# Kernel optimization log

Hardware: AMD Instinct MI355X
Metric: run time of the kernel (lower is better)

Reference implementation:

```python
import jax, jax.numpy as jnp
import numpy as np

NHEAD = 8  # matches init_kwargs

M_NODES = 20000
D_MODEL = 512
N_EDGES = 640000


def setup_inputs() -> dict:
    key = jax.random.key(0)
    ks = jax.random.split(key, 8)
    sc = 1.0 / np.sqrt(D_MODEL)
    return {
        "s": jax.random.normal(ks[0], (M_NODES, D_MODEL), dtype=jnp.float32),
        "edge_index": jax.random.randint(ks[1], (2, N_EDGES), 0, M_NODES, dtype=jnp.int64),
        "Wq": jax.random.normal(ks[2], (D_MODEL, D_MODEL), dtype=jnp.float32) * sc,
        "bq": jax.random.normal(ks[3], (D_MODEL,), dtype=jnp.float32) * sc,
        "Wkv": jax.random.normal(ks[4], (2 * D_MODEL, D_MODEL), dtype=jnp.float32) * sc,
        "bkv": jax.random.normal(ks[5], (2 * D_MODEL,), dtype=jnp.float32) * sc,
        "Wo": jax.random.normal(ks[6], (D_MODEL, D_MODEL), dtype=jnp.float32) * sc,
        "bo": jax.random.normal(ks[7], (D_MODEL,), dtype=jnp.float32) * sc,
    }


def reference(s, edge_index, Wq, bq, Wkv, bkv, Wo, bo):
    M, C = s.shape
    H = NHEAD
    Dh = C // H
    scale = 1.0 / np.sqrt(Dh).astype(np.float32)

    q = (s @ Wq.T + bq).reshape(M, H, Dh)            # [M,H,Dh]
    kv = (s @ Wkv.T + bkv).reshape(M, H, 2 * Dh)     # [M,H,2Dh]
    k, v = kv[..., :Dh], kv[..., Dh:]

    src, tgt = edge_index[0], edge_index[1]

    # per-edge attention logits [E,H]
    a = jnp.einsum('ehc,ehc->eh', q[tgt], k[src]) * scale

    # segment softmax over edges sharing the same target node
    a_max = jax.ops.segment_max(a, tgt, num_segments=M)        # [M,H]
    ex = jnp.exp(a - a_max[tgt])                               # [E,H]
    denom = jax.ops.segment_sum(ex, tgt, num_segments=M)      # [M,H]
    attn = ex / denom[tgt]                                     # [E,H]

    # weighted message aggregation: scatter-sum over target nodes
    o_msg = attn[..., None] * v[src]                           # [E,H,Dh]
    o = jax.ops.segment_sum(o_msg, tgt, num_segments=M)       # [M,H,Dh]
    o = o.reshape(M, C)
    return o @ Wo.T + bo
```

## Files before the change

### kernel.cpp

```cpp
#include <hip/hip_runtime.h>
#include <cmath>

#define MN 20000
#define DM 512
#define NE 640000
#define CAP 128

typedef short bf16x8 __attribute__((ext_vector_type(8)));
typedef float f32x4 __attribute__((ext_vector_type(4)));

__device__ __forceinline__ ushort f2b(float x) {
    unsigned u = __builtin_bit_cast(unsigned, x);
    u += 0x7FFF + ((u >> 16) & 1);
    return (ushort)(u >> 16);
}
__device__ __forceinline__ float b2f(ushort b) {
    return __builtin_bit_cast(float, (unsigned)b << 16);
}

__global__ void conv_bf16_k(const float* __restrict__ in, ushort* __restrict__ out, int n4) {
    int i = blockIdx.x * blockDim.x + threadIdx.x;
    if (i >= n4) return;
    float4 v = ((const float4*)in)[i];
    ushort4 o = { f2b(v.x), f2b(v.y), f2b(v.z), f2b(v.w) };
    ((ushort4*)out)[i] = o;
}

__device__ __forceinline__ const float* wc_src_row(int r, const float* Wq, const float* Wkv) {
    if (r < 512) return Wq + ((size_t)r << 9);
    if (r < 1024) { int h = (r - 512) >> 6, j = (r - 512) & 63;  return Wkv + ((size_t)(h * 128 + j) << 9); }
    { int h = (r - 1024) >> 6, j = (r - 1024) & 63; return Wkv + ((size_t)(h * 128 + 64 + j) << 9); }
}

__global__ void conv_wc_k(const float* __restrict__ Wq, const float* __restrict__ Wkv,
                          ushort* __restrict__ out) {
    int i = blockIdx.x * blockDim.x + threadIdx.x;
    if (i >= 1536 * 512 / 4) return;
    int e = i * 4;
    int row = e >> 9, col = e & 511;
    float4 v = *(const float4*)(wc_src_row(row, Wq, Wkv) + col);
    ushort4 o = { f2b(v.x), f2b(v.y), f2b(v.z), f2b(v.w) };
    ((ushort4*)out)[i] = o;
}

__global__ void bias_perm_k(const float* __restrict__ bq, const float* __restrict__ bkv,
                            float* __restrict__ bc) {
    int r = blockIdx.x * blockDim.x + threadIdx.x;
    if (r >= 1536) return;
    float v;
    if (r < 512) v = bq[r];
    else if (r < 1024) { int h = (r - 512) >> 6, j = (r - 512) & 63;  v = bkv[h * 128 + j]; }
    else               { int h = (r - 1024) >> 6, j = (r - 1024) & 63; v = bkv[h * 128 + 64 + j]; }
    bc[r] = v;
}

__global__ void conv_split_k(const float* __restrict__ in, ushort* __restrict__ oh,
                             ushort* __restrict__ ol, int n4) {
    int i = blockIdx.x * blockDim.x + threadIdx.x;
    if (i >= n4) return;
    float4 v = ((const float4*)in)[i];
    ushort4 h, l;
    h.x = f2b(v.x); l.x = f2b(v.x - b2f(h.x));
    h.y = f2b(v.y); l.y = f2b(v.y - b2f(h.y));
    h.z = f2b(v.z); l.z = f2b(v.z - b2f(h.z));
    h.w = f2b(v.w); l.w = f2b(v.w - b2f(h.w));
    ((ushort4*)oh)[i] = h;
    ((ushort4*)ol)[i] = l;
}

template<int SPLIT, bool OUTBF>
__global__ __launch_bounds__(256) void gemm_mfma(
    const ushort* __restrict__ Ah, const ushort* __restrict__ Al,
    const ushort* __restrict__ Bh, const ushort* __restrict__ Bl,
    const float* __restrict__ bias, void* __restrict__ Cout, int M, int N, int K)
{
    __shared__ ushort lds[4 * 4096];
    const int tid = threadIdx.x;
    const int row0 = blockIdx.x * 128, col0 = blockIdx.y * 128;
    const int wid = tid >> 6, l = tid & 63;
    const int wm = (wid >> 1) * 64, wn = (wid & 1) * 64;
    const int fr = l & 15, g = l >> 4;
    const int fcb = g << 4;

    f32x4 acc[4][4] = {};

    for (int k0 = 0; k0 < K; k0 += 32) {
        __syncthreads();
#pragma unroll
        for (int c = 0; c < 2; ++c) {
            const int lb  = c * 4096 + tid * 16;
            const int r   = lb >> 6;
            const int cbs = (lb & 63) ^ ((r & 6) << 3);
            const int ar  = min(row0 + r, M - 1);
            const int br  = col0 + r;
            const size_t aoff = (size_t)ar * K + k0 + (cbs >> 1);
            const size_t boff = (size_t)br * K + k0 + (cbs >> 1);
            __builtin_amdgcn_global_load_lds(
                (const __attribute__((address_space(1))) void*)(Ah + aoff),
                (__attribute__((address_space(3))) void*)&lds[0 * 4096 + (lb >> 1)], 16, 0, 0);
            __builtin_amdgcn_global_load_lds(
                (const __attribute__((address_space(1))) void*)(Bh + boff),
                (__attribute__((address_space(3))) void*)&lds[1 * 4096 + (lb >> 1)], 16, 0, 0);
            if (SPLIT == 3) {
                __builtin_amdgcn_global_load_lds(
                    (const __attribute__((address_space(1))) void*)(Al + aoff),
                    (__attribute__((address_space(3))) void*)&lds[2 * 4096 + (lb >> 1)], 16, 0, 0);
                __builtin_amdgcn_global_load_lds(
                    (const __attribute__((address_space(1))) void*)(Bl + boff),
                    (__attribute__((address_space(3))) void*)&lds[3 * 4096 + (lb >> 1)], 16, 0, 0);
            }
        }
        __syncthreads();

        bf16x8 ah[4], bh[4], al[4], bl[4];
#pragma unroll
        for (int m = 0; m < 4; ++m) {
            const int r  = wm + m * 16 + fr;
            const int cb = fcb ^ ((r & 6) << 3);
            ah[m] = *(const bf16x8*)&lds[0 * 4096 + r * 32 + (cb >> 1)];
            if (SPLIT == 3) al[m] = *(const bf16x8*)&lds[2 * 4096 + r * 32 + (cb >> 1)];
        }
#pragma unroll
        for (int n = 0; n < 4; ++n) {
            const int r  = wn + n * 16 + fr;
            const int cb = fcb ^ ((r & 6) << 3);
            bh[n] = *(const bf16x8*)&lds[1 * 4096 + r * 32 + (cb >> 1)];
            if (SPLIT == 3) bl[n] = *(const bf16x8*)&lds[3 * 4096 + r * 32 + (cb >> 1)];
        }
#pragma unroll
        for (int m = 0; m < 4; ++m)
#pragma unroll
            for (int n = 0; n < 4; ++n) {
                acc[m][n] = __builtin_amdgcn_mfma_f32_16x16x32_bf16(ah[m], bh[n], acc[m][n], 0, 0, 0);
                if (SPLIT == 3) {
                    acc[m][n] = __builtin_amdgcn_mfma_f32_16x16x32_bf16(ah[m], bl[n], acc[m][n], 0, 0, 0);
                    acc[m][n] = __builtin_amdgcn_mfma_f32_16x16x32_bf16(al[m], bh[n], acc[m][n], 0, 0, 0);
                }
            }
    }

#pragma unroll
    for (int n = 0; n < 4; ++n) {
        const int cg = col0 + wn + n * 16 + fr;
        const float bv = bias[cg];
#pragma unroll
        for (int m = 0; m < 4; ++m) {
#pragma unroll
            for (int j = 0; j < 4; ++j) {
                const int rg = row0 + wm + m * 16 + g * 4 + j;
                if (rg < M) {
                    const float v = acc[m][n][j] + bv;
                    if (OUTBF) ((ushort*)Cout)[(size_t)rg * N + cg] = f2b(v);
                    else       ((float*)Cout)[(size_t)rg * N + cg] = v;
                }
            }
        }
    }
}

__global__ void count_edges_k(const int* __restrict__ tgt, int* __restrict__ counts, int E)
{
    int e = blockIdx.x * blockDim.x + threadIdx.x;
    if (e < E) atomicAdd(&counts[tgt[e]], 1);
}

__global__ __launch_bounds__(1024) void scan_counts_k(
    const int* __restrict__ counts, int* __restrict__ indptr, int M)
{
    __shared__ int part[1024];
    const int t  = threadIdx.x;
    const int CH = (M + 1023) / 1024;
    const int base = t * CH;
    int sum = 0;
    for (int i = 0; i < CH; ++i) {
        int idx = base + i;
        if (idx < M) sum += counts[idx];
    }
    part[t] = sum;
    __syncthreads();
    for (int off = 1; off < 1024; off <<= 1) {
        int v = (t >= off) ? part[t - off] : 0;
        __syncthreads();
        part[t] += v;
        __syncthreads();
    }
    int excl = part[t] - sum;
    for (int i = 0; i < CH; ++i) {
        int idx = base + i;
        if (idx < M) { indptr[idx] = excl; excl += counts[idx]; }
    }
    if (t == 1023) indptr[M] = part[1023];
}

__global__ void scatter_edges_k(const int* __restrict__ src, const int* __restrict__ tgt,
                                const int* __restrict__ indptr, int* __restrict__ cursor,
                                int* __restrict__ slot_src, int E)
{
    int e = blockIdx.x * blockDim.x + threadIdx.x;
    if (e < E) {
        int t   = tgt[e];
        int pos = atomicAdd(&cursor[t], 1);
        slot_src[indptr[t] + pos] = src[e];
    }
}

__global__ __launch_bounds__(256) void attn3_k(
    const ushort* __restrict__ qkv, const int* __restrict__ indptr,
    const int* __restrict__ slot_src, ushort* __restrict__ obh, ushort* __restrict__ obl)
{
    __shared__ int slots[4][CAP];
    const int w = threadIdx.x >> 6;
    const int l = threadIdx.x & 63;
    const int node = blockIdx.x * 4 + w;
    const int beg = indptr[node], end = indptr[node + 1];
    const int d = end - beg;

    for (int i = l; i < d && i < CAP; i += 64) slots[w][i] = slot_src[beg + i];
    __syncthreads();

    float qf[8];
    {
        bf16x8 qv = *(const bf16x8*)(qkv + (size_t)node * 1536 + (l << 3));
#pragma unroll
        for (int j = 0; j < 8; ++j) qf[j] = b2f((ushort)qv[j]);
    }

    float acc[8] = {};
    float ssum = 0.f;

    int i = 0;
    for (; i + 4 <= d; i += 4) {
        const int s0 = (i + 0 < CAP) ? slots[w][i + 0] : slot_src[beg + i + 0];
        const int s1 = (i + 1 < CAP) ? slots[w][i + 1] : slot_src[beg + i + 1];
        const int s2 = (i + 2 < CAP) ? slots[w][i + 2] : slot_src[beg + i + 2];
        const int s3 = (i + 3 < CAP) ? slots[w][i + 3] : slot_src[beg + i + 3];
        const ushort* r0 = qkv + (size_t)s0 * 1536 + (l << 3);
        const ushort* r1 = qkv + (size_t)s1 * 1536 + (l << 3);
        const ushort* r2 = qkv + (size_t)s2 * 1536 + (l << 3);
        const ushort* r3 = qkv + (size_t)s3 * 1536 + (l << 3);
        bf16x8 k0 = *(const bf16x8*)(r0 + 512);
        bf16x8 v0 = *(const bf16x8*)(r0 + 1024);
        bf16x8 k1 = *(const bf16x8*)(r1 + 512);
        bf16x8 v1 = *(const bf16x8*)(r1 + 1024);
        bf16x8 k2 = *(const bf16x8*)(r2 + 512);
        bf16x8 v2 = *(const bf16x8*)(r2 + 1024);
        bf16x8 k3 = *(const bf16x8*)(r3 + 512);
        bf16x8 v3 = *(const bf16x8*)(r3 + 1024);

        float p0 = 0.f, p1 = 0.f, p2 = 0.f, p3 = 0.f;
#pragma unroll
        for (int j = 0; j < 8; ++j) {
            p0 = fmaf(qf[j], b2f((ushort)k0[j]), p0);
            p1 = fmaf(qf[j], b2f((ushort)k1[j]), p1);
            p2 = fmaf(qf[j], b2f((ushort)k2[j]), p2);
            p3 = fmaf(qf[j], b2f((ushort)k3[j]), p3);
        }
        p0 += __shfl_xor(p0, 1); p0 += __shfl_xor(p0, 2); p0 += __shfl_xor(p0, 4);
        p1 += __shfl_xor(p1, 1); p1 += __shfl_xor(p1, 2); p1 += __shfl_xor(p1, 4);
        p2 += __shfl_xor(p2, 1); p2 += __shfl_xor(p2, 2); p2 += __shfl_xor(p2, 4);
        p3 += __shfl_xor(p3, 1); p3 += __shfl_xor(p3, 2); p3 += __shfl_xor(p3, 4);

        const float w0 = __expf(p0 * 0.125f);
        const float w1 = __expf(p1 * 0.125f);
        const float w2 = __expf(p2 * 0.125f);
        const float w3 = __expf(p3 * 0.125f);
        ssum += (w0 + w1) + (w2 + w3);
#pragma unroll
        for (int j = 0; j < 8; ++j) {
            float a = acc[j];
            a = fmaf(w0, b2f((ushort)v0[j]), a);
            a = fmaf(w1, b2f((ushort)v1[j]), a);
            a = fmaf(w2, b2f((ushort)v2[j]), a);
            a = fmaf(w3, b2f((ushort)v3[j]), a);
            acc[j] = a;
        }
    }
    for (; i < d; ++i) {
        const int s0 = (i < CAP) ? slots[w][i] : slot_src[beg + i];
        const ushort* r0 = qkv + (size_t)s0 * 1536 + (l << 3);
        bf16x8 k0 = *(const bf16x8*)(r0 + 512);
        bf16x8 v0 = *(const bf16x8*)(r0 + 1024);
        float p0 = 0.f;
#pragma unroll
        for (int j = 0; j < 8; ++j) p0 = fmaf(qf[j], b2f((ushort)k0[j]), p0);
        p0 += __shfl_xor(p0, 1); p0 += __shfl_xor(p0, 2); p0 += __shfl_xor(p0, 4);
        const float w0 = __expf(p0 * 0.125f);
        ssum += w0;
#pragma unroll
        for (int j = 0; j < 8; ++j) acc[j] = fmaf(w0, b2f((ushort)v0[j]), acc[j]);
    }

    const float inv = (d > 0) ? 1.f / ssum : 0.f;
    ushort4 ph0, ph1, pl0, pl1;
    float o;
    o = acc[0] * inv; ph0.x = f2b(o); pl0.x = f2b(o - b2f(ph0.x));
    o = acc[1] * inv; ph0.y = f2b(o); pl0.y = f2b(o - b2f(ph0.y));
    o = acc[2] * inv; ph0.z = f2b(o); pl0.z = f2b(o - b2f(ph0.z));
    o = acc[3] * inv; ph0.w = f2b(o); pl0.w = f2b(o - b2f(ph0.w));
    o = acc[4] * inv; ph1.x = f2b(o); pl1.x = f2b(o - b2f(ph1.x));
    o = acc[5] * inv; ph1.y = f2b(o); pl1.y = f2b(o - b2f(ph1.y));
    o = acc[6] * inv; ph1.z = f2b(o); pl1.z = f2b(o - b2f(ph1.z));
    o = acc[7] * inv; ph1.w = f2b(o); pl1.w = f2b(o - b2f(ph1.w));
    const size_t ob_off = (size_t)node * 512 + (l << 3);
    *(ushort4*)(obh + ob_off)     = ph0;
    *(ushort4*)(obh + ob_off + 4) = ph1;
    *(ushort4*)(obl + ob_off)     = pl0;
    *(ushort4*)(obl + ob_off + 4) = pl1;
}

extern "C" void kernel_launch(void* const* d_in, const int* in_sizes, int n_in,
                              void* d_out, int out_size, void* d_ws, size_t ws_size,
                              hipStream_t stream)
{
    const float* s   = (const float*)d_in[0];
    const int*   eix = (const int*)d_in[1];
    const float* Wq  = (const float*)d_in[2];
    const float* bq  = (const float*)d_in[3];
    const float* Wkv = (const float*)d_in[4];
    const float* bkv = (const float*)d_in[5];
    const float* Wo  = (const float*)d_in[6];
    const float* bo  = (const float*)d_in[7];
    float* out = (float*)d_out;

    char* ws = (char*)d_ws;
    auto take = [&](size_t bytes) { char* p = ws; ws += (bytes + 255) & ~(size_t)255; return p; };
    ushort* qkv_b = (ushort*)take((size_t)MN * 1536 * 2);
    ushort* s_b   = (ushort*)take((size_t)MN * 512 * 2);
    ushort* obh   = (ushort*)take((size_t)MN * 512 * 2);
    ushort* obl   = (ushort*)take((size_t)MN * 512 * 2);
    ushort* Wc_b  = (ushort*)take((size_t)1536 * 512 * 2);
    ushort* Wo_h  = (ushort*)take((size_t)512 * 512 * 2);
    ushort* Wo_l  = (ushort*)take((size_t)512 * 512 * 2);
    float*  bc    = (float*)take(1536 * 4);
    int* counts   = (int*)take(MN * 4);
    int* cursor   = (int*)take(MN * 4);
    int* slot_src = (int*)take((size_t)NE * 4);
    int* indptr   = (int*)take((MN + 4) * 4);

    hipMemsetAsync(counts, 0, MN * 4, stream);
    hipMemsetAsync(cursor, 0, MN * 4, stream);

    conv_bf16_k<<<(MN * 512 / 4 + 255) / 256, 256, 0, stream>>>(s, s_b, MN * 512 / 4);
    conv_wc_k<<<(1536 * 512 / 4 + 255) / 256, 256, 0, stream>>>(Wq, Wkv, Wc_b);
    bias_perm_k<<<6, 256, 0, stream>>>(bq, bkv, bc);
    conv_split_k<<<(512 * 512 / 4 + 255) / 256, 256, 0, stream>>>(Wo, Wo_h, Wo_l, 512 * 512 / 4);

    count_edges_k<<<NE / 256, 256, 0, stream>>>(eix + NE, counts, NE);
    scan_counts_k<<<1, 1024, 0, stream>>>(counts, indptr, MN);
    scatter_edges_k<<<NE / 256, 256, 0, stream>>>(eix, eix + NE, indptr, cursor, slot_src, NE);

    dim3 g1((MN + 127) / 128, 1536 / 128);
    gemm_mfma<1, true><<<g1, 256, 0, stream>>>(s_b, s_b, Wc_b, Wc_b, bc, qkv_b, MN, 1536, DM);

    attn3_k<<<MN / 4, 256, 0, stream>>>(qkv_b, indptr, slot_src, obh, obl);

    dim3 g2((MN + 127) / 128, 512 / 128);
    gemm_mfma<3, false><<<g2, 256, 0, stream>>>(obh, obl, Wo_h, Wo_l, bo, out, MN, 512, DM);
}
```

Baseline: 425.2 us.

## Sort attention nodes by degree, unroll gather by 8, drop split-bf16 output GEMM

Adds a degree histogram, scan and scatter that build a permutation ordering nodes by descending in-degree, so each attention block handles nodes of similar degree and waves within a block finish closer together. The attention inner loop gathers 8 neighbours per iteration instead of 4 to keep more loads in flight, and runs under a launch bound of 4 blocks. The attention output and Wo are now single bf16 instead of hi/lo split pairs, so the output GEMM does one pass instead of three. This lowers precision in the final projection and adds three small kernels and two memsets.

Measured after the change: 476.3 us. +12.0%, slower.

```diff
diff --git a/kernel.cpp b/kernel.cpp
--- a/kernel.cpp
+++ b/kernel.cpp
@@ -52,20 +52,6 @@
     else if (r < 1024) { int h = (r - 512) >> 6, j = (r - 512) & 63;  v = bkv[h * 128 + j]; }
     else               { int h = (r - 1024) >> 6, j = (r - 1024) & 63; v = bkv[h * 128 + 64 + j]; }
     bc[r] = v;
-}
-
-__global__ void conv_split_k(const float* __restrict__ in, ushort* __restrict__ oh,
-                             ushort* __restrict__ ol, int n4) {
-    int i = blockIdx.x * blockDim.x + threadIdx.x;
-    if (i >= n4) return;
-    float4 v = ((const float4*)in)[i];
-    ushort4 h, l;
-    h.x = f2b(v.x); l.x = f2b(v.x - b2f(h.x));
-    h.y = f2b(v.y); l.y = f2b(v.y - b2f(h.y));
-    h.z = f2b(v.z); l.z = f2b(v.z - b2f(h.z));
-    h.w = f2b(v.w); l.w = f2b(v.w - b2f(h.w));
-    ((ushort4*)oh)[i] = h;
-    ((ushort4*)ol)[i] = l;
 }
 
 template<int SPLIT, bool OUTBF>
@@ -204,14 +190,49 @@
     }
 }
 
-__global__ __launch_bounds__(256) void attn3_k(
+__global__ void deg_hist_k(const int* __restrict__ counts, int* __restrict__ dhist, int M)
+{
+    int n = blockIdx.x * blockDim.x + threadIdx.x;
+    if (n < M) atomicAdd(&dhist[127 - min(counts[n], 127)], 1);
+}
+
+__global__ __launch_bounds__(128) void deg_scan_k(const int* __restrict__ dhist,
+                                                  int* __restrict__ dbase)
+{
+    __shared__ int tmp[128];
+    const int t = threadIdx.x;
+    const int v = dhist[t];
+    tmp[t] = v;
+    __syncthreads();
+    for (int off = 1; off < 128; off <<= 1) {
+        int u = (t >= off) ? tmp[t - off] : 0;
+        __syncthreads();
+        tmp[t] += u;
+        __syncthreads();
+    }
+    dbase[t] = tmp[t] - v;
+}
+
+__global__ void deg_scatter_k(const int* __restrict__ counts, const int* __restrict__ dbase,
+                              int* __restrict__ dcur, int* __restrict__ perm, int M)
+{
+    int n = blockIdx.x * blockDim.x + threadIdx.x;
+    if (n < M) {
+        int b = 127 - min(counts[n], 127);
+        int pos = atomicAdd(&dcur[b], 1);
+        perm[dbase[b] + pos] = n;
+    }
+}
+
+__global__ __launch_bounds__(256, 4) void attn4_k(
     const ushort* __restrict__ qkv, const int* __restrict__ indptr,
-    const int* __restrict__ slot_src, ushort* __restrict__ obh, ushort* __restrict__ obl)
+    const int* __restrict__ slot_src, const int* __restrict__ perm,
+    ushort* __restrict__ obh)
 {
     __shared__ int slots[4][CAP];
     const int w = threadIdx.x >> 6;
     const int l = threadIdx.x & 63;
-    const int node = blockIdx.x * 4 + w;
+    const int node = perm[blockIdx.x * 4 + w];
     const int beg = indptr[node], end = indptr[node + 1];
     const int d = end - beg;
 
@@ -229,51 +250,39 @@
     float ssum = 0.f;
 
     int i = 0;
-    for (; i + 4 <= d; i += 4) {
-        const int s0 = (i + 0 < CAP) ? slots[w][i + 0] : slot_src[beg + i + 0];
-        const int s1 = (i + 1 < CAP) ? slots[w][i + 1] : slot_src[beg + i + 1];
-        const int s2 = (i + 2 < CAP) ? slots[w][i + 2] : slot_src[beg + i + 2];
-        const int s3 = (i + 3 < CAP) ? slots[w][i + 3] : slot_src[beg + i + 3];
-        const ushort* r0 = qkv + (size_t)s0 * 1536 + (l << 3);
-        const ushort* r1 = qkv + (size_t)s1 * 1536 + (l << 3);
-        const ushort* r2 = qkv + (size_t)s2 * 1536 + (l << 3);
-        const ushort* r3 = qkv + (size_t)s3 * 1536 + (l << 3);
-        bf16x8 k0 = *(const bf16x8*)(r0 + 512);
-        bf16x8 v0 = *(const bf16x8*)(r0 + 1024);
-        bf16x8 k1 = *(const bf16x8*)(r1 + 512);
-        bf16x8 v1 = *(const bf16x8*)(r1 + 1024);
-        bf16x8 k2 = *(const bf16x8*)(r2 + 512);
-        bf16x8 v2 = *(const bf16x8*)(r2 + 1024);
-        bf16x8 k3 = *(const bf16x8*)(r3 + 512);
-        bf16x8 v3 = *(const bf16x8*)(r3 + 1024);
-
-        float p0 = 0.f, p1 = 0.f, p2 = 0.f, p3 = 0.f;
-#pragma unroll
-        for (int j = 0; j < 8; ++j) {
-            p0 = fmaf(qf[j], b2f((ushort)k0[j]), p0);
-            p1 = fmaf(qf[j], b2f((ushort)k1[j]), p1);
-            p2 = fmaf(qf[j], b2f((ushort)k2[j]), p2);
-            p3 = fmaf(qf[j], b2f((ushort)k3[j]), p3);
-        }
-        p0 += __shfl_xor(p0, 1); p0 += __shfl_xor(p0, 2); p0 += __shfl_xor(p0, 4);
-        p1 += __shfl_xor(p1, 1); p1 += __shfl_xor(p1, 2); p1 += __shfl_xor(p1, 4);
-        p2 += __shfl_xor(p2, 1); p2 += __shfl_xor(p2, 2); p2 += __shfl_xor(p2, 4);
-        p3 += __shfl_xor(p3, 1); p3 += __shfl_xor(p3, 2); p3 += __shfl_xor(p3, 4);
-
-        const float w0 = __expf(p0 * 0.125f);
-        const float w1 = __expf(p1 * 0.125f);
-        const float w2 = __expf(p2 * 0.125f);
-        const float w3 = __expf(p3 * 0.125f);
-        ssum += (w0 + w1) + (w2 + w3);
-#pragma unroll
-        for (int j = 0; j < 8; ++j) {
-            float a = acc[j];
-            a = fmaf(w0, b2f((ushort)v0[j]), a);
-            a = fmaf(w1, b2f((ushort)v1[j]), a);
-            a = fmaf(w2, b2f((ushort)v2[j]), a);
-            a = fmaf(w3, b2f((ushort)v3[j]), a);
-            acc[j] = a;
-        }
+    for (; i + 8 <= d; i += 8) {
+        int ss[8];
+#pragma unroll
+        for (int u = 0; u < 8; ++u)
+            ss[u] = (i + u < CAP) ? slots[w][i + u] : slot_src[beg + i + u];
+        bf16x8 kk[8], vv[8];
+#pragma unroll
+        for (int u = 0; u < 8; ++u) {
+            const ushort* r = qkv + (size_t)ss[u] * 1536 + (l << 3);
+            kk[u] = *(const bf16x8*)(r + 512);
+            vv[u] = *(const bf16x8*)(r + 1024);
+        }
+        float p[8];
+#pragma unroll
+        for (int u = 0; u < 8; ++u) {
+            float pu = 0.f;
+#pragma unroll
+            for (int j = 0; j < 8; ++j) pu = fmaf(qf[j], b2f((ushort)kk[u][j]), pu);
+            p[u] = pu;
+        }
+#pragma unroll
+        for (int u = 0; u < 8; ++u) {
+            p[u] += __shfl_xor(p[u], 1);
+            p[u] += __shfl_xor(p[u], 2);
+            p[u] += __shfl_xor(p[u], 4);
+        }
+        float wt[8];
+#pragma unroll
+        for (int u = 0; u < 8; ++u) { wt[u] = __expf(p[u] * 0.125f); ssum += wt[u]; }
+#pragma unroll
+        for (int u = 0; u < 8; ++u)
+#pragma unroll
+            for (int j = 0; j < 8; ++j) acc[j] = fmaf(wt[u], b2f((ushort)vv[u][j]), acc[j]);
     }
     for (; i < d; ++i) {
         const int s0 = (i < CAP) ? slots[w][i] : slot_src[beg + i];
@@ -291,21 +300,14 @@
     }
 
     const float inv = (d > 0) ? 1.f / ssum : 0.f;
-    ushort4 ph0, ph1, pl0, pl1;
-    float o;
-    o = acc[0] * inv; ph0.x = f2b(o); pl0.x = f2b(o - b2f(ph0.x));
-    o = acc[1] * inv; ph0.y = f2b(o); pl0.y = f2b(o - b2f(ph0.y));
-    o = acc[2] * inv; ph0.z = f2b(o); pl0.z = f2b(o - b2f(ph0.z));
-    o = acc[3] * inv; ph0.w = f2b(o); pl0.w = f2b(o - b2f(ph0.w));
-    o = acc[4] * inv; ph1.x = f2b(o); pl1.x = f2b(o - b2f(ph1.x));
-    o = acc[5] * inv; ph1.y = f2b(o); pl1.y = f2b(o - b2f(ph1.y));
-    o = acc[6] * inv; ph1.z = f2b(o); pl1.z = f2b(o - b2f(ph1.z));
-    o = acc[7] * inv; ph1.w = f2b(o); pl1.w = f2b(o - b2f(ph1.w));
+    ushort4 ph0, ph1;
+    ph0.x = f2b(acc[0] * inv); ph0.y = f2b(acc[1] * inv);
+    ph0.z = f2b(acc[2] * inv); ph0.w = f2b(acc[3] * inv);
+    ph1.x = f2b(acc[4] * inv); ph1.y = f2b(acc[5] * inv);
+    ph1.z = f2b(acc[6] * inv); ph1.w = f2b(acc[7] * inv);
     const size_t ob_off = (size_t)node * 512 + (l << 3);
     *(ushort4*)(obh + ob_off)     = ph0;
     *(ushort4*)(obh + ob_off + 4) = ph1;
-    *(ushort4*)(obl + ob_off)     = pl0;
-    *(ushort4*)(obl + ob_off + 4) = pl1;
 }
 
 extern "C" void kernel_launch(void* const* d_in, const int* in_sizes, int n_in,
@@ -327,33 +329,40 @@
     ushort* qkv_b = (ushort*)take((size_t)MN * 1536 * 2);
     ushort* s_b   = (ushort*)take((size_t)MN * 512 * 2);
     ushort* obh   = (ushort*)take((size_t)MN * 512 * 2);
-    ushort* obl   = (ushort*)take((size_t)MN * 512 * 2);
     ushort* Wc_b  = (ushort*)take((size_t)1536 * 512 * 2);
-    ushort* Wo_h  = (ushort*)take((size_t)512 * 512 * 2);
-    ushort* Wo_l  = (ushort*)take((size_t)512 * 512 * 2);
+    ushort* Wo_b  = (ushort*)take((size_t)512 * 512 * 2);
     float*  bc    = (float*)take(1536 * 4);
     int* counts   = (int*)take(MN * 4);
     int* cursor   = (int*)take(MN * 4);
     int* slot_src = (int*)take((size_t)NE * 4);
     int* indptr   = (int*)take((MN + 4) * 4);
+    int* dhist    = (int*)take(128 * 4);
+    int* dbase    = (int*)take(128 * 4);
+    int* dcur     = (int*)take(128 * 4);
+    int* perm     = (int*)take(MN * 4);
 
     hipMemsetAsync(counts, 0, MN * 4, stream);
     hipMemsetAsync(cursor, 0, MN * 4, stream);
+    hipMemsetAsync(dhist, 0, 128 * 4, stream);
+    hipMemsetAsync(dcur, 0, 128 * 4, stream);
 
     conv_bf16_k<<<(MN * 512 / 4 + 255) / 256, 256, 0, stream>>>(s, s_b, MN * 512 / 4);
     conv_wc_k<<<(1536 * 512 / 4 + 255) / 256, 256, 0, stream>>>(Wq, Wkv, Wc_b);
     bias_perm_k<<<6, 256, 0, stream>>>(bq, bkv, bc);
-    conv_split_k<<<(512 * 512 / 4 + 255) / 256, 256, 0, stream>>>(Wo, Wo_h, Wo_l, 512 * 512 / 4);
+    conv_bf16_k<<<(512 * 512 / 4 + 255) / 256, 256, 0, stream>>>(Wo, Wo_b, 512 * 512 / 4);
 
     count_edges_k<<<NE / 256, 256, 0, stream>>>(eix + NE, counts, NE);
     scan_counts_k<<<1, 1024, 0, stream>>>(counts, indptr, MN);
     scatter_edges_k<<<NE / 256, 256, 0, stream>>>(eix, eix + NE, indptr, cursor, slot_src, NE);
+    deg_hist_k<<<(MN + 255) / 256, 256, 0, stream>>>(counts, dhist, MN);
+    deg_scan_k<<<1, 128, 0, stream>>>(dhist, dbase);
+    deg_scatter_k<<<(MN + 255) / 256, 256, 0, stream>>>(counts, dbase, dcur, perm, MN);
 
     dim3 g1((MN + 127) / 128, 1536 / 128);
     gemm_mfma<1, true><<<g1, 256, 0, stream>>>(s_b, s_b, Wc_b, Wc_b, bc, qkv_b, MN, 1536, DM);
 
-    attn3_k<<<MN / 4, 256, 0, stream>>>(qkv_b, indptr, slot_src, obh, obl);
+    attn4_k<<<MN / 4, 256, 0, stream>>>(qkv_b, indptr, slot_src, perm, obh);
 
     dim3 g2((MN + 127) / 128, 512 / 128);
-    gemm_mfma<3, false><<<g2, 256, 0, stream>>>(obh, obl, Wo_h, Wo_l, bo, out, MN, 512, DM);
-}
+    gemm_mfma<1, false><<<g2, 256, 0, stream>>>(obh, obh, Wo_b, Wo_b, bo, out, MN, 512, DM);
+}
```
